# Kernel tuning notes

Hardware: AMD Instinct MI355X
Metric: run time of the kernel (lower is better)

## Reference

```python
import jax, jax.numpy as jnp
import numpy as np

D_MODEL = 1024
NUM_HEAD = 16
BATCH = 2
SEQ = 2048
NEG_INF = -1e9  # matches masked_fill value in the original


def setup_inputs() -> dict:
    key = jax.random.key(0)
    k1, k2, k3, k4, k5 = jax.random.split(key, 5)
    scale = 1.0 / np.sqrt(D_MODEL)
    return {
        "x": jax.random.normal(k1, (BATCH, SEQ, D_MODEL), dtype=jnp.float32),
        "q_weight": jax.random.normal(k2, (D_MODEL, D_MODEL), dtype=jnp.float32) * scale,
        "k_weight": jax.random.normal(k3, (D_MODEL, D_MODEL), dtype=jnp.float32) * scale,
        "v_weight": jax.random.normal(k4, (D_MODEL, D_MODEL), dtype=jnp.float32) * scale,
        "o_weight": jax.random.normal(k5, (D_MODEL, D_MODEL), dtype=jnp.float32) * scale,
    }


def reference(x, q_weight, k_weight, v_weight, o_weight):
    b, s, d = x.shape
    h = NUM_HEAD
    dh = d // h
    # projections: weight layout is (d_out, d_in)
    q = jnp.einsum('bsd,ed->bse', x, q_weight).reshape(b, s, h, dh).transpose(0, 2, 1, 3)
    k = jnp.einsum('bsd,ed->bse', x, k_weight).reshape(b, s, h, dh).transpose(0, 2, 1, 3)
    v = jnp.einsum('bsd,ed->bse', x, v_weight).reshape(b, s, h, dh).transpose(0, 2, 1, 3)
    scores = jnp.einsum('bhqd,bhkd->bhqk', q, k) / jnp.sqrt(jnp.asarray(dh, x.dtype))
    causal = jnp.triu(jnp.ones((s, s), dtype=bool), k=1)  # True above diagonal -> masked
    scores = jnp.where(causal, jnp.asarray(NEG_INF, x.dtype), scores)
    attn = jax.nn.softmax(scores, axis=-1)
    out = jnp.einsum('bhqk,bhkd->bhqd', attn, v)          # [b,h,s,dh]
    out = out.transpose(0, 2, 1, 3).reshape(b, s, d)       # merge heads
    return jnp.einsum('bse,de->bsd', out, o_weight)
```

## Files before the change

kernel.cpp:

```cpp
#include <hip/hip_runtime.h>

typedef short bhalf8 __attribute__((ext_vector_type(8)));
typedef float floatx4 __attribute__((ext_vector_type(4)));

#define D_MODEL 1024
#define SEQ     2048
#define BATCH   2
#define NHEAD   16
#define DH      64

#define GLDS(g, l) __builtin_amdgcn_global_load_lds( \
    (const __attribute__((address_space(1))) void*)(g), \
    (__attribute__((address_space(3))) void*)(l), 16, 0, 0)

static __device__ __forceinline__ short f2bf(float f) {
    unsigned u = __builtin_bit_cast(unsigned, f);
    u = (u + 0x7fffu + ((u >> 16) & 1u)) >> 16;
    return (short)u;
}
static __device__ __forceinline__ unsigned pack2(float a, float b) {
    return (unsigned)(unsigned short)f2bf(a) | ((unsigned)(unsigned short)f2bf(b) << 16);
}

__global__ __launch_bounds__(256) void cast_x(const float* __restrict__ s,
                                              short* __restrict__ d) {
    int i = (blockIdx.x * 256 + threadIdx.x) * 8;
    float4 a = *(const float4*)(s + i);
    float4 b = *(const float4*)(s + i + 4);
    uint4 u = {pack2(a.x, a.y), pack2(a.z, a.w), pack2(b.x, b.y), pack2(b.z, b.w)};
    *(uint4*)(d + i) = u;
}

__global__ __launch_bounds__(256) void cast_w(const float* __restrict__ wq,
                                              const float* __restrict__ wk,
                                              const float* __restrict__ wv,
                                              const float* __restrict__ wo,
                                              short* __restrict__ dst) {
    const float* s = (blockIdx.y == 0) ? wq : (blockIdx.y == 1) ? wk
                   : (blockIdx.y == 2) ? wv : wo;
    size_t off = (size_t)blockIdx.y * (D_MODEL * D_MODEL);
    int i = (blockIdx.x * 256 + threadIdx.x) * 8;
    float4 a = *(const float4*)(s + i);
    float4 b = *(const float4*)(s + i + 4);
    uint4 u = {pack2(a.x, a.y), pack2(a.z, a.w), pack2(b.x, b.y), pack2(b.z, b.w)};
    *(uint4*)(dst + off + i) = u;
}

__global__ __launch_bounds__(256) void gemm_qkv(const short* __restrict__ A,
                                                const short* __restrict__ W,
                                                short* __restrict__ Qo,
                                                short* __restrict__ Ko,
                                                short* __restrict__ Vt) {
    __shared__ __align__(16) char pool[34816];
    short (*As)[64] = (short(*)[64])pool;
    short (*Bs)[64] = (short(*)[64])(pool + 16384);
    const int t    = threadIdx.x;
    const int wave = t >> 6, lane = t & 63, quad = lane >> 4, l16 = lane & 15;
    const int bm = blockIdx.x * 128, by = blockIdx.y, bn = by * 128;
    const int qm = (wave >> 1) * 64, qn = (wave & 1) * 64;

    const int lrow = lane >> 3, lcol = (lane & 7) * 8;
    const short* Ag = A + (size_t)(bm + wave * 32 + lrow) * 1024 + lcol;
    const short* Wg = W + (size_t)(bn + wave * 32 + lrow) * 1024 + lcol;
    short* Al = &As[wave * 32][0];
    short* Bl = &Bs[wave * 32][0];

    floatx4 acc[4][4];
#pragma unroll
    for (int i = 0; i < 4; ++i)
#pragma unroll
        for (int j = 0; j < 4; ++j) {
            floatx4 z = {0.f, 0.f, 0.f, 0.f};
            acc[i][j] = z;
        }

    for (int k0 = 0; k0 < 1024; k0 += 64) {
        __syncthreads();
#pragma unroll
        for (int j = 0; j < 4; ++j) {
            GLDS(Ag + k0 + (size_t)j * 8 * 1024, Al + j * 8 * 64);
            GLDS(Wg + k0 + (size_t)j * 8 * 1024, Bl + j * 8 * 64);
        }
        __syncthreads();
#pragma unroll
        for (int kk = 0; kk < 64; kk += 32) {
            bhalf8 af[4], bfr[4];
#pragma unroll
            for (int im = 0; im < 4; ++im)
                af[im] = *(const bhalf8*)&As[qm + im * 16 + l16][kk + quad * 8];
#pragma unroll
            for (int jn = 0; jn < 4; ++jn)
                bfr[jn] = *(const bhalf8*)&Bs[qn + jn * 16 + l16][kk + quad * 8];
#pragma unroll
            for (int im = 0; im < 4; ++im)
#pragma unroll
                for (int jn = 0; jn < 4; ++jn)
                    acc[im][jn] = __builtin_amdgcn_mfma_f32_16x16x32_bf16(
                        af[im], bfr[jn], acc[im][jn], 0, 0, 0);
        }
    }

    __syncthreads();
    short (*Ct)[136] = (short(*)[136])pool;
    const bool isV = (by >= 16);
#pragma unroll
    for (int im = 0; im < 4; ++im)
#pragma unroll
        for (int jn = 0; jn < 4; ++jn)
#pragma unroll
            for (int g = 0; g < 4; ++g) {
                const int ml = qm + im * 16 + quad * 4 + g;
                const int nl = qn + jn * 16 + l16;
                if (isV) Ct[nl][ml] = f2bf(acc[im][jn][g]);
                else     Ct[ml][nl] = f2bf(acc[im][jn][g]);
            }
    __syncthreads();

    short* outp;
    size_t rowbase, colbase, stride;
    if (by < 8)       { outp = Qo; rowbase = bm;                colbase = bn;        stride = 1024; }
    else if (by < 16) { outp = Ko; rowbase = bm;                colbase = bn - 1024; stride = 1024; }
    else              { outp = Vt; rowbase = (size_t)bn - 2048; colbase = bm;        stride = 4096; }
#pragma unroll
    for (int pass = 0; pass < 8; ++pass) {
        const int r = (t >> 4) + pass * 16;
        const int c = (t & 15) * 8;
        uint4 u = *(const uint4*)&Ct[r][c];
        *(uint4*)(outp + (rowbase + r) * stride + colbase + c) = u;
    }
}

__global__ __launch_bounds__(256) void gemm_o(const short* __restrict__ A,
                                              const short* __restrict__ W,
                                              float* __restrict__ C) {
    __shared__ __align__(16) char pool[34816];
    short (*As)[64] = (short(*)[64])pool;
    short (*Bs)[64] = (short(*)[64])(pool + 16384);
    const int t    = threadIdx.x;
    const int wave = t >> 6, lane = t & 63, quad = lane >> 4, l16 = lane & 15;
    const int bm = blockIdx.x * 128, bn = blockIdx.y * 64;
    const int qm = (wave >> 1) * 64, qn = (wave & 1) * 32;

    const int lrow = lane >> 3, lcol = (lane & 7) * 8;
    const short* Ag = A + (size_t)(bm + wave * 32 + lrow) * 1024 + lcol;
    const short* Wg = W + (size_t)(bn + wave * 16 + lrow) * 1024 + lcol;
    short* Al = &As[wave * 32][0];
    short* Bl = &Bs[wave * 16][0];

    floatx4 acc[4][2];
#pragma unroll
    for (int i = 0; i < 4; ++i)
#pragma unroll
        for (int j = 0; j < 2; ++j) {
            floatx4 z = {0.f, 0.f, 0.f, 0.f};
            acc[i][j] = z;
        }

    for (int k0 = 0; k0 < 1024; k0 += 64) {
        __syncthreads();
#pragma unroll
        for (int j = 0; j < 4; ++j)
            GLDS(Ag + k0 + (size_t)j * 8 * 1024, Al + j * 8 * 64);
#pragma unroll
        for (int j = 0; j < 2; ++j)
            GLDS(Wg + k0 + (size_t)j * 8 * 1024, Bl + j * 8 * 64);
        __syncthreads();
#pragma unroll
        for (int kk = 0; kk < 64; kk += 32) {
            bhalf8 af[4], bfr[2];
#pragma unroll
            for (int im = 0; im < 4; ++im)
                af[im] = *(const bhalf8*)&As[qm + im * 16 + l16][kk + quad * 8];
#pragma unroll
            for (int jn = 0; jn < 2; ++jn)
                bfr[jn] = *(const bhalf8*)&Bs[qn + jn * 16 + l16][kk + quad * 8];
#pragma unroll
            for (int im = 0; im < 4; ++im)
#pragma unroll
                for (int jn = 0; jn < 2; ++jn)
                    acc[im][jn] = __builtin_amdgcn_mfma_f32_16x16x32_bf16(
                        af[im], bfr[jn], acc[im][jn], 0, 0, 0);
        }
    }

    __syncthreads();
    float (*Ctf)[68] = (float(*)[68])pool;
#pragma unroll
    for (int im = 0; im < 4; ++im)
#pragma unroll
        for (int jn = 0; jn < 2; ++jn)
#pragma unroll
            for (int g = 0; g < 4; ++g)
                Ctf[qm + im * 16 + quad * 4 + g][qn + jn * 16 + l16] = acc[im][jn][g];
    __syncthreads();
#pragma unroll
    for (int pass = 0; pass < 8; ++pass) {
        const int r = (t >> 4) + pass * 16;
        const int c = (t & 15) * 4;
        float4 u = *(const float4*)&Ctf[r][c];
        *(float4*)(C + (size_t)(bm + r) * 1024 + bn + c) = u;
    }
}

__global__ __launch_bounds__(512) void attn_v7(const short* __restrict__ Qo,
                                               const short* __restrict__ Ko,
                                               const short* __restrict__ Vt,
                                               short* __restrict__ Y) {
    __shared__ __align__(16) short Ps[8][32][72];
    const int t    = threadIdx.x;
    const int wave = t >> 6, lane = t & 63, quad = lane >> 4, l16 = lane & 15;
    const int bh = blockIdx.x, b = bh >> 4, h = bh & 15;
    const int qtile = (wave < 4) ? (15 - (int)blockIdx.y) : (int)blockIdx.y;
    const int qw = qtile * 128 + (wave & 3) * 32;

    const short* Qbase = Qo + (size_t)b * SEQ * 1024 + h * 64;
    const short* Kbase = Ko + (size_t)b * SEQ * 1024 + h * 64;
    const short* Vbase = Vt + (size_t)h * 64 * 4096 + (size_t)b * SEQ;

    bhalf8 qf[2][2];
#pragma unroll
    for (int im = 0; im < 2; ++im) {
        const short* qr = Qbase + (size_t)(qw + im * 16 + l16) * 1024;
        qf[im][0] = *(const bhalf8*)(qr + quad * 8);
        qf[im][1] = *(const bhalf8*)(qr + 32 + quad * 8);
    }

    float lsum[2][4];
    floatx4 o[2][4];
#pragma unroll
    for (int im = 0; im < 2; ++im)
#pragma unroll
        for (int g = 0; g < 4; ++g) lsum[im][g] = 0.f;
#pragma unroll
    for (int im = 0; im < 2; ++im)
#pragma unroll
        for (int nd = 0; nd < 4; ++nd) {
            floatx4 z = {0.f, 0.f, 0.f, 0.f};
            o[im][nd] = z;
        }

    const float KS = 0.125f * 1.44269504f;
    const float CB = 12.0f * 1.44269504f;

    for (int k0 = 0; k0 < qw + 32; k0 += 64) {
        bhalf8 kf[4][2];
#pragma unroll
        for (int jn = 0; jn < 4; ++jn) {
            const short* kr = Kbase + (size_t)(k0 + jn * 16 + l16) * 1024 + quad * 8;
            kf[jn][0] = *(const bhalf8*)(kr);
            kf[jn][1] = *(const bhalf8*)(kr + 32);
        }
        bhalf8 vt[4][2];
#pragma unroll
        for (int nd = 0; nd < 4; ++nd) {
            const short* vr = Vbase + (size_t)(nd * 16 + l16) * 4096 + k0 + quad * 8;
            vt[nd][0] = *(const bhalf8*)(vr);
            vt[nd][1] = *(const bhalf8*)(vr + 32);
        }

        floatx4 s[2][4];
#pragma unroll
        for (int im = 0; im < 2; ++im)
#pragma unroll
            for (int jn = 0; jn < 4; ++jn) {
                floatx4 z = {0.f, 0.f, 0.f, 0.f};
                z = __builtin_amdgcn_mfma_f32_16x16x32_bf16(qf[im][0], kf[jn][0], z, 0, 0, 0);
                z = __builtin_amdgcn_mfma_f32_16x16x32_bf16(qf[im][1], kf[jn][1], z, 0, 0, 0);
                s[im][jn] = z;
            }

        const bool partial = (k0 + 64 > qw);
#pragma unroll
        for (int im = 0; im < 2; ++im)
#pragma unroll
            for (int g = 0; g < 4; ++g) {
                const int rr = im * 16 + quad * 4 + g;
                const int qrow = qw + rr;
                float e0 = exp2f(s[im][0][g] * KS - CB);
                float e1 = exp2f(s[im][1][g] * KS - CB);
                float e2 = exp2f(s[im][2][g] * KS - CB);
                float e3 = exp2f(s[im][3][g] * KS - CB);
                if (partial) {
                    if (k0 + l16 > qrow)      e0 = 0.f;
                    if (k0 + 16 + l16 > qrow) e1 = 0.f;
                    if (k0 + 32 + l16 > qrow) e2 = 0.f;
                    if (k0 + 48 + l16 > qrow) e3 = 0.f;
                }
                lsum[im][g] += (e0 + e1) + (e2 + e3);
                Ps[wave][rr][l16]      = f2bf(e0);
                Ps[wave][rr][16 + l16] = f2bf(e1);
                Ps[wave][rr][32 + l16] = f2bf(e2);
                Ps[wave][rr][48 + l16] = f2bf(e3);
            }

#pragma unroll
        for (int im = 0; im < 2; ++im) {
            bhalf8 ap0 = *(const bhalf8*)&Ps[wave][im * 16 + l16][quad * 8];
            bhalf8 ap1 = *(const bhalf8*)&Ps[wave][im * 16 + l16][32 + quad * 8];
#pragma unroll
            for (int nd = 0; nd < 4; ++nd) {
                o[im][nd] = __builtin_amdgcn_mfma_f32_16x16x32_bf16(ap0, vt[nd][0], o[im][nd], 0, 0, 0);
                o[im][nd] = __builtin_amdgcn_mfma_f32_16x16x32_bf16(ap1, vt[nd][1], o[im][nd], 0, 0, 0);
            }
        }
    }

    float inv[2][4];
#pragma unroll
    for (int im = 0; im < 2; ++im)
#pragma unroll
        for (int g = 0; g < 4; ++g) {
            float r = lsum[im][g];
            r += __shfl_xor(r, 1, 64);
            r += __shfl_xor(r, 2, 64);
            r += __shfl_xor(r, 4, 64);
            r += __shfl_xor(r, 8, 64);
            inv[im][g] = 1.0f / r;
        }
#pragma unroll
    for (int im = 0; im < 2; ++im)
#pragma unroll
        for (int nd = 0; nd < 4; ++nd)
#pragma unroll
            for (int g = 0; g < 4; ++g) {
                const int qrow = qw + im * 16 + quad * 4 + g;
                Y[(size_t)(b * SEQ + qrow) * 1024 + h * 64 + nd * 16 + l16] =
                    f2bf(o[im][nd][g] * inv[im][g]);
            }
}

extern "C" void kernel_launch(void* const* d_in, const int* in_sizes, int n_in,
                              void* d_out, int out_size, void* d_ws, size_t ws_size,
                              hipStream_t stream) {
    const float* x  = (const float*)d_in[0];
    const float* wq = (const float*)d_in[1];
    const float* wk = (const float*)d_in[2];
    const float* wv = (const float*)d_in[3];
    const float* wo = (const float*)d_in[4];

    short* xb   = (short*)d_ws;
    short* Qo   = xb + (size_t)4096 * 1024;
    short* Ko   = Qo + (size_t)4096 * 1024;
    short* Vt   = Ko + (size_t)4096 * 1024;
    short* wall = Vt + (size_t)1024 * 4096;
    short* wob  = wall + (size_t)3 * 1024 * 1024;

    cast_x<<<dim3(2048), 256, 0, stream>>>(x, xb);
    cast_w<<<dim3(512, 4), 256, 0, stream>>>(wq, wk, wv, wo, wall);
    gemm_qkv<<<dim3(32, 24), 256, 0, stream>>>(xb, wall, Qo, Ko, Vt);
    attn_v7<<<dim3(BATCH * NHEAD, 8), 512, 0, stream>>>(Qo, Ko, Vt, xb);
    gemm_o<<<dim3(32, 16), 256, 0, stream>>>(xb, wob, (float*)d_out);
}
```

Measured before the change: 220.8 us.

## Rebalance causal attention work across waves with split-K merge and prefetching

Each wave pair now handles a high and a low 32-row query strip. Waves A process the first 17 key chunks of the high strip. Waves B process the low strip plus the remaining chunks of the high strip, and partial outputs and sums are merged through shared memory. This evens out per-wave causal work, which was skewed before. K/V fragments are also prefetched one chunk ahead, and bf16 packing uses the hardware cvt_pk instruction. The costs are extra register pressure, a block-wide sync with an LDS combine, and more complex indexing.

Measured after the change: 221.9 us. Within noise of the previous version (+0.5%).

```diff
diff --git a/kernel.cpp b/kernel.cpp
--- a/kernel.cpp
+++ b/kernel.cpp
@@ -20,6 +20,11 @@
 }
 static __device__ __forceinline__ unsigned pack2(float a, float b) {
     return (unsigned)(unsigned short)f2bf(a) | ((unsigned)(unsigned short)f2bf(b) << 16);
+}
+static __device__ __forceinline__ unsigned cvt_pk_bf16(float lo, float hi) {
+    unsigned r;
+    asm("v_cvt_pk_bf16_f32 %0, %1, %2" : "=v"(r) : "v"(lo), "v"(hi));
+    return r;
 }
 
 __global__ __launch_bounds__(256) void cast_x(const float* __restrict__ s,
@@ -202,131 +207,215 @@
     }
 }
 
-__global__ __launch_bounds__(512) void attn_v7(const short* __restrict__ Qo,
+#define LOADQ(qf, qwv) do {                                                   \
+    _Pragma("unroll")                                                         \
+    for (int im_ = 0; im_ < 2; ++im_) {                                       \
+        const short* qr_ = Qbase + (size_t)((qwv) + im_ * 16 + l16) * 1024;   \
+        qf[im_][0] = *(const bhalf8*)(qr_ + quad * 8);                        \
+        qf[im_][1] = *(const bhalf8*)(qr_ + 32 + quad * 8);                   \
+    } } while (0)
+
+#define LOADK(dst, kk) do {                                                   \
+    _Pragma("unroll")                                                         \
+    for (int jn_ = 0; jn_ < 4; ++jn_) {                                       \
+        const short* kr_ = Kbase + (size_t)((kk) + jn_ * 16 + l16) * 1024 + quad * 8; \
+        dst[jn_][0] = *(const bhalf8*)(kr_);                                  \
+        dst[jn_][1] = *(const bhalf8*)(kr_ + 32);                             \
+    } } while (0)
+
+#define LOADV(dst, kk) do {                                                   \
+    _Pragma("unroll")                                                         \
+    for (int nd_ = 0; nd_ < 4; ++nd_) {                                       \
+        const short* vr_ = Vbase + (size_t)(nd_ * 16 + l16) * 4096 + (kk) + quad * 8; \
+        dst[nd_][0] = *(const bhalf8*)(vr_);                                  \
+        dst[nd_][1] = *(const bhalf8*)(vr_ + 32);                             \
+    } } while (0)
+
+#define ZERO_ACC() do {                                                       \
+    _Pragma("unroll")                                                         \
+    for (int im_ = 0; im_ < 2; ++im_) {                                       \
+        _Pragma("unroll")                                                     \
+        for (int g_ = 0; g_ < 4; ++g_) lsum[im_][g_] = 0.f;                   \
+        _Pragma("unroll")                                                     \
+        for (int nd_ = 0; nd_ < 4; ++nd_) {                                   \
+            floatx4 z_ = {0.f, 0.f, 0.f, 0.f};                                \
+            o[im_][nd_] = z_;                                                 \
+        }                                                                     \
+    } } while (0)
+
+#define CHUNK(k0v, knv, qf, qwv) do {                                         \
+    floatx4 s_[2][4];                                                         \
+    _Pragma("unroll")                                                         \
+    for (int im_ = 0; im_ < 2; ++im_)                                         \
+        _Pragma("unroll")                                                     \
+        for (int jn_ = 0; jn_ < 4; ++jn_) {                                   \
+            floatx4 z_ = {0.f, 0.f, 0.f, 0.f};                                \
+            z_ = __builtin_amdgcn_mfma_f32_16x16x32_bf16(qf[im_][0], kf[jn_][0], z_, 0, 0, 0); \
+            z_ = __builtin_amdgcn_mfma_f32_16x16x32_bf16(qf[im_][1], kf[jn_][1], z_, 0, 0, 0); \
+            s_[im_][jn_] = z_;                                                \
+        }                                                                     \
+    LOADK(kf, knv);                                \
+    const bool partial_ = ((k0v) + 64 > (qwv));                               \
+    _Pragma("unroll")                                                         \
+    for (int im_ = 0; im_ < 2; ++im_)                                         \
+        _Pragma("unroll")                                                     \
+        for (int g_ = 0; g_ < 4; ++g_) {                                      \
+            const int rr_ = im_ * 16 + quad * 4 + g_;                         \
+            const int qrow_ = (qwv) + rr_;                                    \
+            float e0_ = exp2f(s_[im_][0][g_] * KS - CB);                      \
+            float e1_ = exp2f(s_[im_][1][g_] * KS - CB);                      \
+            float e2_ = exp2f(s_[im_][2][g_] * KS - CB);                      \
+            float e3_ = exp2f(s_[im_][3][g_] * KS - CB);                      \
+            if (partial_) {                                                   \
+                if ((k0v) + l16 > qrow_)      e0_ = 0.f;                      \
+                if ((k0v) + 16 + l16 > qrow_) e1_ = 0.f;                      \
+                if ((k0v) + 32 + l16 > qrow_) e2_ = 0.f;                      \
+                if ((k0v) + 48 + l16 > qrow_) e3_ = 0.f;                      \
+            }                                                                 \
+            lsum[im_][g_] += (e0_ + e1_) + (e2_ + e3_);                       \
+            unsigned r01_ = cvt_pk_bf16(e0_, e1_);                            \
+            unsigned r23_ = cvt_pk_bf16(e2_, e3_);                            \
+            Ps[wave][rr_][l16]      = (short)r01_;                            \
+            Ps[wave][rr_][16 + l16] = (short)(r01_ >> 16);                    \
+            Ps[wave][rr_][32 + l16] = (short)r23_;                            \
+            Ps[wave][rr_][48 + l16] = (short)(r23_ >> 16);                    \
+        }                                                                     \
+    _Pragma("unroll")                                                         \
+    for (int im_ = 0; im_ < 2; ++im_) {                                       \
+        bhalf8 ap0_ = *(const bhalf8*)&Ps[wave][im_ * 16 + l16][quad * 8];    \
+        bhalf8 ap1_ = *(const bhalf8*)&Ps[wave][im_ * 16 + l16][32 + quad * 8]; \
+        _Pragma("unroll")                                                     \
+        for (int nd_ = 0; nd_ < 4; ++nd_) {                                   \
+            o[im_][nd_] = __builtin_amdgcn_mfma_f32_16x16x32_bf16(ap0_, vt[nd_][0], o[im_][nd_], 0, 0, 0); \
+            o[im_][nd_] = __builtin_amdgcn_mfma_f32_16x16x32_bf16(ap1_, vt[nd_][1], o[im_][nd_], 0, 0, 0); \
+        }                                                                     \
+    }                                                                         \
+    LOADV(vt, knv);                                     \
+} while (0)
+
+#define RUN_SEG(nseg, kbase, qf, qwv) do {                                    \
+    const int n_ = (nseg);                                                    \
+    const int base_ = (kbase);                                                \
+    if (n_ > 0) {                                                             \
+        LOADK(kf, base_);                                                     \
+        LOADV(vt, base_);                                                     \
+        _Pragma("unroll 1")                                                   \
+        for (int i_ = 0; i_ < n_; ++i_) {                                     \
+            const int k0_ = base_ + i_ * 64;                                  \
+            const int kn_ = (i_ + 1 < n_) ? (k0_ + 64) : base_;               \
+            CHUNK(k0_, kn_, qf, qwv);                                         \
+        }                                                                     \
+    } } while (0)
+
+#define REDUCE_LSUM() do {                                                    \
+    _Pragma("unroll")                                                         \
+    for (int im_ = 0; im_ < 2; ++im_)                                         \
+        _Pragma("unroll")                                                     \
+        for (int g_ = 0; g_ < 4; ++g_) {                                      \
+            float r_ = lsum[im_][g_];                                         \
+            r_ += __shfl_xor(r_, 1, 64);                                      \
+            r_ += __shfl_xor(r_, 2, 64);                                      \
+            r_ += __shfl_xor(r_, 4, 64);                                      \
+            r_ += __shfl_xor(r_, 8, 64);                                      \
+            lsum[im_][g_] = r_;                                               \
+        } } while (0)
+
+#define STORE_OUT(qwv) do {                                                   \
+    _Pragma("unroll")                                                         \
+    for (int im_ = 0; im_ < 2; ++im_)                                         \
+        _Pragma("unroll")                                                     \
+        for (int g_ = 0; g_ < 4; ++g_) {                                      \
+            const float iv_ = 1.0f / lsum[im_][g_];                           \
+            const int qrow_ = (qwv) + im_ * 16 + quad * 4 + g_;               \
+            _Pragma("unroll")                                                 \
+            for (int nd_ = 0; nd_ < 4; ++nd_)                                 \
+                Y[(size_t)(b * SEQ + qrow_) * 1024 + h * 64 + nd_ * 16 + l16] = \
+                    f2bf(o[im_][nd_][g_] * iv_);                              \
+        } } while (0)
+
+__global__ __launch_bounds__(512) void attn_v8(const short* __restrict__ Qo,
                                                const short* __restrict__ Ko,
                                                const short* __restrict__ Vt,
                                                short* __restrict__ Y) {
-    __shared__ __align__(16) short Ps[8][32][72];
+    __shared__ __align__(16) char pool[45056];
+    short (*Ps)[32][72] = (short(*)[32][72])pool;
+    float (*Cmb)[44]    = (float(*)[44])pool;
+
     const int t    = threadIdx.x;
     const int wave = t >> 6, lane = t & 63, quad = lane >> 4, l16 = lane & 15;
     const int bh = blockIdx.x, b = bh >> 4, h = bh & 15;
-    const int qtile = (wave < 4) ? (15 - (int)blockIdx.y) : (int)blockIdx.y;
-    const int qw = qtile * 128 + (wave & 3) * 32;
+    const bool isA = (wave < 4);
+    const int j   = (int)blockIdx.y * 4 + (wave & 3);
+    const int sH  = 63 - j;
+    const int qwH = sH * 32, qwL = j * 32;
+    const int ncH = (65 - j) >> 1;
+    const int ncL = (j + 2) >> 1;
 
     const short* Qbase = Qo + (size_t)b * SEQ * 1024 + h * 64;
     const short* Kbase = Ko + (size_t)b * SEQ * 1024 + h * 64;
     const short* Vbase = Vt + (size_t)h * 64 * 4096 + (size_t)b * SEQ;
 
-    bhalf8 qf[2][2];
-#pragma unroll
-    for (int im = 0; im < 2; ++im) {
-        const short* qr = Qbase + (size_t)(qw + im * 16 + l16) * 1024;
-        qf[im][0] = *(const bhalf8*)(qr + quad * 8);
-        qf[im][1] = *(const bhalf8*)(qr + 32 + quad * 8);
-    }
-
+    const float KS = 0.125f * 1.44269504f;
+    const float CB = 12.0f * 1.44269504f;
+
+    bhalf8 kf[4][2], vt[4][2];
     float lsum[2][4];
     floatx4 o[2][4];
-#pragma unroll
-    for (int im = 0; im < 2; ++im)
-#pragma unroll
-        for (int g = 0; g < 4; ++g) lsum[im][g] = 0.f;
-#pragma unroll
-    for (int im = 0; im < 2; ++im)
-#pragma unroll
-        for (int nd = 0; nd < 4; ++nd) {
-            floatx4 z = {0.f, 0.f, 0.f, 0.f};
-            o[im][nd] = z;
-        }
-
-    const float KS = 0.125f * 1.44269504f;
-    const float CB = 12.0f * 1.44269504f;
-
-    for (int k0 = 0; k0 < qw + 32; k0 += 64) {
-        bhalf8 kf[4][2];
-#pragma unroll
-        for (int jn = 0; jn < 4; ++jn) {
-            const short* kr = Kbase + (size_t)(k0 + jn * 16 + l16) * 1024 + quad * 8;
-            kf[jn][0] = *(const bhalf8*)(kr);
-            kf[jn][1] = *(const bhalf8*)(kr + 32);
-        }
-        bhalf8 vt[4][2];
-#pragma unroll
-        for (int nd = 0; nd < 4; ++nd) {
-            const short* vr = Vbase + (size_t)(nd * 16 + l16) * 4096 + k0 + quad * 8;
-            vt[nd][0] = *(const bhalf8*)(vr);
-            vt[nd][1] = *(const bhalf8*)(vr + 32);
-        }
-
-        floatx4 s[2][4];
+    ZERO_ACC();
+
+    if (isA) {
+        bhalf8 qfH[2][2];
+        LOADQ(qfH, qwH);
+        RUN_SEG(17, 0, qfH, qwH);
+        REDUCE_LSUM();
+    } else {
+        {
+            bhalf8 qfL[2][2];
+            LOADQ(qfL, qwL);
+            RUN_SEG(ncL, 0, qfL, qwL);
+            REDUCE_LSUM();
+            STORE_OUT(qwL);
+        }
+        ZERO_ACC();
+        {
+            bhalf8 qfH[2][2];
+            LOADQ(qfH, qwH);
+            RUN_SEG(ncH - 17, 1088, qfH, qwH);
+            REDUCE_LSUM();
+        }
+    }
+
+    __syncthreads();
+    if (!isA) {
+        float* cp = &Cmb[(wave - 4) * 64 + lane][0];
 #pragma unroll
         for (int im = 0; im < 2; ++im)
 #pragma unroll
-            for (int jn = 0; jn < 4; ++jn) {
-                floatx4 z = {0.f, 0.f, 0.f, 0.f};
-                z = __builtin_amdgcn_mfma_f32_16x16x32_bf16(qf[im][0], kf[jn][0], z, 0, 0, 0);
-                z = __builtin_amdgcn_mfma_f32_16x16x32_bf16(qf[im][1], kf[jn][1], z, 0, 0, 0);
-                s[im][jn] = z;
+            for (int nd = 0; nd < 4; ++nd)
+                *(floatx4*)(cp + (im * 4 + nd) * 4) = o[im][nd];
+#pragma unroll
+        for (int im = 0; im < 2; ++im)
+#pragma unroll
+            for (int g = 0; g < 4; ++g)
+                cp[32 + im * 4 + g] = lsum[im][g];
+    }
+    __syncthreads();
+    if (isA) {
+        const float* cp = &Cmb[wave * 64 + lane][0];
+#pragma unroll
+        for (int im = 0; im < 2; ++im)
+#pragma unroll
+            for (int nd = 0; nd < 4; ++nd) {
+                floatx4 add = *(const floatx4*)(cp + (im * 4 + nd) * 4);
+                o[im][nd] += add;
             }
-
-        const bool partial = (k0 + 64 > qw);
 #pragma unroll
         for (int im = 0; im < 2; ++im)
 #pragma unroll
-            for (int g = 0; g < 4; ++g) {
-                const int rr = im * 16 + quad * 4 + g;
-                const int qrow = qw + rr;
-                float e0 = exp2f(s[im][0][g] * KS - CB);
-                float e1 = exp2f(s[im][1][g] * KS - CB);
-                float e2 = exp2f(s[im][2][g] * KS - CB);
-                float e3 = exp2f(s[im][3][g] * KS - CB);
-                if (partial) {
-                    if (k0 + l16 > qrow)      e0 = 0.f;
-                    if (k0 + 16 + l16 > qrow) e1 = 0.f;
-                    if (k0 + 32 + l16 > qrow) e2 = 0.f;
-                    if (k0 + 48 + l16 > qrow) e3 = 0.f;
-                }
-                lsum[im][g] += (e0 + e1) + (e2 + e3);
-                Ps[wave][rr][l16]      = f2bf(e0);
-                Ps[wave][rr][16 + l16] = f2bf(e1);
-                Ps[wave][rr][32 + l16] = f2bf(e2);
-                Ps[wave][rr][48 + l16] = f2bf(e3);
-            }
-
-#pragma unroll
-        for (int im = 0; im < 2; ++im) {
-            bhalf8 ap0 = *(const bhalf8*)&Ps[wave][im * 16 + l16][quad * 8];
-            bhalf8 ap1 = *(const bhalf8*)&Ps[wave][im * 16 + l16][32 + quad * 8];
-#pragma unroll
-            for (int nd = 0; nd < 4; ++nd) {
-                o[im][nd] = __builtin_amdgcn_mfma_f32_16x16x32_bf16(ap0, vt[nd][0], o[im][nd], 0, 0, 0);
-                o[im][nd] = __builtin_amdgcn_mfma_f32_16x16x32_bf16(ap1, vt[nd][1], o[im][nd], 0, 0, 0);
-            }
-        }
-    }
-
-    float inv[2][4];
-#pragma unroll
-    for (int im = 0; im < 2; ++im)
-#pragma unroll
-        for (int g = 0; g < 4; ++g) {
-            float r = lsum[im][g];
-            r += __shfl_xor(r, 1, 64);
-            r += __shfl_xor(r, 2, 64);
-            r += __shfl_xor(r, 4, 64);
-            r += __shfl_xor(r, 8, 64);
-            inv[im][g] = 1.0f / r;
-        }
-#pragma unroll
-    for (int im = 0; im < 2; ++im)
-#pragma unroll
-        for (int nd = 0; nd < 4; ++nd)
-#pragma unroll
-            for (int g = 0; g < 4; ++g) {
-                const int qrow = qw + im * 16 + quad * 4 + g;
-                Y[(size_t)(b * SEQ + qrow) * 1024 + h * 64 + nd * 16 + l16] =
-                    f2bf(o[im][nd][g] * inv[im][g]);
-            }
+            for (int g = 0; g < 4; ++g)
+                lsum[im][g] += cp[32 + im * 4 + g];
+        STORE_OUT(qwH);
+    }
 }
 
 extern "C" void kernel_launch(void* const* d_in, const int* in_sizes, int n_in,
@@ -348,6 +437,6 @@
     cast_x<<<dim3(2048), 256, 0, stream>>>(x, xb);
     cast_w<<<dim3(512, 4), 256, 0, stream>>>(wq, wk, wv, wo, wall);
     gemm_qkv<<<dim3(32, 24), 256, 0, stream>>>(xb, wall, Qo, Ko, Vt);
-    attn_v7<<<dim3(BATCH * NHEAD, 8), 512, 0, stream>>>(Qo, Ko, Vt, xb);
+    attn_v8<<<dim3(BATCH * NHEAD, 8), 512, 0, stream>>>(Qo, Ko, Vt, xb);
     gemm_o<<<dim3(32, 16), 256, 0, stream>>>(xb, wob, (float*)d_out);
 }
```

## Stage K/V tiles in double-buffered LDS shared by all waves in attention

Applied to the files above, without the earlier changes.

The attention kernel is restructured so that each block's 8 waves cooperatively load each 64-key K and V chunk into double-buffered shared memory, with register prefetch two chunks ahead. Before, every wave read K and V directly from global memory. Each wave now handles 16 query rows instead of 32, and the block processes two query tiles one after the other (a long one and a short one) to balance causal work. The probability packing uses the hardware v_cvt_pk_bf16_f32 instruction. In exchange, the kernel adds a barrier per chunk and lowers per-wave MFMA reuse of K and V fragments.

New measurement: 204.2 us. -7.5%, faster.

```diff
diff --git a/kernel.cpp b/kernel.cpp
--- a/kernel.cpp
+++ b/kernel.cpp
@@ -20,6 +20,11 @@
 }
 static __device__ __forceinline__ unsigned pack2(float a, float b) {
     return (unsigned)(unsigned short)f2bf(a) | ((unsigned)(unsigned short)f2bf(b) << 16);
+}
+static __device__ __forceinline__ unsigned cvt_pk_bf16(float lo, float hi) {
+    unsigned r;
+    asm("v_cvt_pk_bf16_f32 %0, %1, %2" : "=v"(r) : "v"(lo), "v"(hi));
+    return r;
 }
 
 __global__ __launch_bounds__(256) void cast_x(const float* __restrict__ s,
@@ -202,131 +207,143 @@
     }
 }
 
-__global__ __launch_bounds__(512) void attn_v7(const short* __restrict__ Qo,
-                                               const short* __restrict__ Ko,
-                                               const short* __restrict__ Vt,
-                                               short* __restrict__ Y) {
-    __shared__ __align__(16) short Ps[8][32][72];
+#define MFMA_BF16 __builtin_amdgcn_mfma_f32_16x16x32_bf16
+
+#define STAGE_LOAD(kregv, vregv, kk) do {                                     \
+    kregv = *(const uint4*)(Kbase + (size_t)((kk) + sr) * 1024 + sc);         \
+    vregv = *(const uint4*)(Vbase + (size_t)sr * 4096 + (kk) + sc);           \
+    } while (0)
+
+#define STAGE_WRITE(bufv, kregv, vregv) do {                                  \
+    *(uint4*)&Ks[bufv][sr][sc] = kregv;                                       \
+    *(uint4*)&Vs[bufv][sr][sc] = vregv;                                       \
+    } while (0)
+
+#define CHUNK13(bufv, k0v, qwv) do {                                          \
+    bhalf8 kf_[4][2];                                                         \
+    _Pragma("unroll")                                                         \
+    for (int jn_ = 0; jn_ < 4; ++jn_) {                                       \
+        kf_[jn_][0] = *(const bhalf8*)&Ks[bufv][jn_ * 16 + l16][quad * 8];    \
+        kf_[jn_][1] = *(const bhalf8*)&Ks[bufv][jn_ * 16 + l16][32 + quad * 8]; \
+    }                                                                         \
+    floatx4 s_[4];                                                            \
+    _Pragma("unroll")                                                         \
+    for (int jn_ = 0; jn_ < 4; ++jn_) {                                       \
+        floatx4 z_ = {0.f, 0.f, 0.f, 0.f};                                    \
+        z_ = MFMA_BF16(qf0, kf_[jn_][0], z_, 0, 0, 0);                        \
+        z_ = MFMA_BF16(qf1, kf_[jn_][1], z_, 0, 0, 0);                        \
+        s_[jn_] = z_;                                                         \
+    }                                                                         \
+    bhalf8 vf_[4][2];              \
+    _Pragma("unroll")                                                         \
+    for (int nd_ = 0; nd_ < 4; ++nd_) {                                       \
+        vf_[nd_][0] = *(const bhalf8*)&Vs[bufv][nd_ * 16 + l16][quad * 8];    \
+        vf_[nd_][1] = *(const bhalf8*)&Vs[bufv][nd_ * 16 + l16][32 + quad * 8]; \
+    }                                                                         \
+    const bool partial_ = ((k0v) + 64 > (qwv));                               \
+    _Pragma("unroll")                                                         \
+    for (int g_ = 0; g_ < 4; ++g_) {                                          \
+        const int rr_ = quad * 4 + g_;                                        \
+        const int qrow_ = (qwv) + rr_;                                        \
+        float e0_ = exp2f(s_[0][g_] * KS - CB);                               \
+        float e1_ = exp2f(s_[1][g_] * KS - CB);                               \
+        float e2_ = exp2f(s_[2][g_] * KS - CB);                               \
+        float e3_ = exp2f(s_[3][g_] * KS - CB);                               \
+        if (partial_) {                                                       \
+            if ((k0v) + l16 > qrow_)      e0_ = 0.f;                          \
+            if ((k0v) + 16 + l16 > qrow_) e1_ = 0.f;                          \
+            if ((k0v) + 32 + l16 > qrow_) e2_ = 0.f;                          \
+            if ((k0v) + 48 + l16 > qrow_) e3_ = 0.f;                          \
+        }                                                                     \
+        lsum[g_] += (e0_ + e1_) + (e2_ + e3_);                                \
+        unsigned r01_ = cvt_pk_bf16(e0_, e1_);                                \
+        unsigned r23_ = cvt_pk_bf16(e2_, e3_);                                \
+        Ps[wave][rr_][l16]      = (short)r01_;                                \
+        Ps[wave][rr_][16 + l16] = (short)(r01_ >> 16);                        \
+        Ps[wave][rr_][32 + l16] = (short)r23_;                                \
+        Ps[wave][rr_][48 + l16] = (short)(r23_ >> 16);                        \
+    }                                                                         \
+          \
+    bhalf8 ap0_ = *(const bhalf8*)&Ps[wave][l16][quad * 8];                   \
+    bhalf8 ap1_ = *(const bhalf8*)&Ps[wave][l16][32 + quad * 8];              \
+    _Pragma("unroll")                                                         \
+    for (int nd_ = 0; nd_ < 4; ++nd_) {                                       \
+        o[nd_] = MFMA_BF16(ap0_, vf_[nd_][0], o[nd_], 0, 0, 0);               \
+        o[nd_] = MFMA_BF16(ap1_, vf_[nd_][1], o[nd_], 0, 0, 0);               \
+    }                                                                         \
+} while (0)
+
+#define SWEEP(qtv, ncv) do {                                                  \
+    const int qw_ = (qtv) * 128 + wave * 16;                                  \
+    const short* qr_ = Qbase + (size_t)(qw_ + l16) * 1024;                    \
+    bhalf8 qf0 = *(const bhalf8*)(qr_ + quad * 8);                            \
+    bhalf8 qf1 = *(const bhalf8*)(qr_ + 32 + quad * 8);                       \
+    _Pragma("unroll")                                                         \
+    for (int g_ = 0; g_ < 4; ++g_) lsum[g_] = 0.f;                            \
+    _Pragma("unroll")                                                         \
+    for (int nd_ = 0; nd_ < 4; ++nd_) {                                       \
+        floatx4 z_ = {0.f, 0.f, 0.f, 0.f};                                    \
+        o[nd_] = z_;                                                          \
+    }                                                                         \
+    uint4 kreg_, vreg_;                                                       \
+    STAGE_LOAD(kreg_, vreg_, 0);                                              \
+    STAGE_WRITE(0, kreg_, vreg_);                                             \
+    if ((ncv) > 1) STAGE_LOAD(kreg_, vreg_, 64);                              \
+    __syncthreads();                                                          \
+    _Pragma("unroll 1")                                                       \
+    for (int i_ = 0; i_ < (ncv); ++i_) {                                      \
+        const int buf_ = i_ & 1;                                              \
+        if (i_ + 1 < (ncv)) STAGE_WRITE(buf_ ^ 1, kreg_, vreg_);              \
+        if (i_ + 2 < (ncv)) STAGE_LOAD(kreg_, vreg_, (i_ + 2) * 64);          \
+        CHUNK13(buf_, i_ * 64, qw_);                                          \
+        __syncthreads();                                                      \
+    }                                                                         \
+    _Pragma("unroll")                                                         \
+    for (int g_ = 0; g_ < 4; ++g_) {                                          \
+        float r_ = lsum[g_];                                                  \
+        r_ += __shfl_xor(r_, 1, 64);                                          \
+        r_ += __shfl_xor(r_, 2, 64);                                          \
+        r_ += __shfl_xor(r_, 4, 64);                                          \
+        r_ += __shfl_xor(r_, 8, 64);                                          \
+        const float iv_ = 1.0f / r_;                                          \
+        const int qrow_ = qw_ + quad * 4 + g_;                                \
+        _Pragma("unroll")                                                     \
+        for (int nd_ = 0; nd_ < 4; ++nd_)                                     \
+            Y[(size_t)(b * SEQ + qrow_) * 1024 + h * 64 + nd_ * 16 + l16] =   \
+                f2bf(o[nd_][g_] * iv_);                                       \
+    }                                                                         \
+} while (0)
+
+__global__ __launch_bounds__(512) void attn_v13(const short* __restrict__ Qo,
+                                                const short* __restrict__ Ko,
+                                                const short* __restrict__ Vt,
+                                                short* __restrict__ Y) {
+    __shared__ __align__(16) short Ks[2][64][72];
+    __shared__ __align__(16) short Vs[2][64][72];
+    __shared__ __align__(16) short Ps[8][16][72];
+
     const int t    = threadIdx.x;
     const int wave = t >> 6, lane = t & 63, quad = lane >> 4, l16 = lane & 15;
-    const int bh = blockIdx.x, b = bh >> 4, h = bh & 15;
-    const int qtile = (wave < 4) ? (15 - (int)blockIdx.y) : (int)blockIdx.y;
-    const int qw = qtile * 128 + (wave & 3) * 32;
+    const int bid  = (int)blockIdx.x;
+    const int bh   = bid & 31, pair = bid >> 5;
+    const int b = bh >> 4, h = bh & 15;
+    const int qtA = 15 - pair, qtB = pair;
 
     const short* Qbase = Qo + (size_t)b * SEQ * 1024 + h * 64;
     const short* Kbase = Ko + (size_t)b * SEQ * 1024 + h * 64;
     const short* Vbase = Vt + (size_t)h * 64 * 4096 + (size_t)b * SEQ;
 
-    bhalf8 qf[2][2];
-#pragma unroll
-    for (int im = 0; im < 2; ++im) {
-        const short* qr = Qbase + (size_t)(qw + im * 16 + l16) * 1024;
-        qf[im][0] = *(const bhalf8*)(qr + quad * 8);
-        qf[im][1] = *(const bhalf8*)(qr + 32 + quad * 8);
-    }
-
-    float lsum[2][4];
-    floatx4 o[2][4];
-#pragma unroll
-    for (int im = 0; im < 2; ++im)
-#pragma unroll
-        for (int g = 0; g < 4; ++g) lsum[im][g] = 0.f;
-#pragma unroll
-    for (int im = 0; im < 2; ++im)
-#pragma unroll
-        for (int nd = 0; nd < 4; ++nd) {
-            floatx4 z = {0.f, 0.f, 0.f, 0.f};
-            o[im][nd] = z;
-        }
+    const int sr = t >> 3;
+    const int sc = (t & 7) * 8;
 
     const float KS = 0.125f * 1.44269504f;
     const float CB = 12.0f * 1.44269504f;
 
-    for (int k0 = 0; k0 < qw + 32; k0 += 64) {
-        bhalf8 kf[4][2];
-#pragma unroll
-        for (int jn = 0; jn < 4; ++jn) {
-            const short* kr = Kbase + (size_t)(k0 + jn * 16 + l16) * 1024 + quad * 8;
-            kf[jn][0] = *(const bhalf8*)(kr);
-            kf[jn][1] = *(const bhalf8*)(kr + 32);
-        }
-        bhalf8 vt[4][2];
-#pragma unroll
-        for (int nd = 0; nd < 4; ++nd) {
-            const short* vr = Vbase + (size_t)(nd * 16 + l16) * 4096 + k0 + quad * 8;
-            vt[nd][0] = *(const bhalf8*)(vr);
-            vt[nd][1] = *(const bhalf8*)(vr + 32);
-        }
-
-        floatx4 s[2][4];
-#pragma unroll
-        for (int im = 0; im < 2; ++im)
-#pragma unroll
-            for (int jn = 0; jn < 4; ++jn) {
-                floatx4 z = {0.f, 0.f, 0.f, 0.f};
-                z = __builtin_amdgcn_mfma_f32_16x16x32_bf16(qf[im][0], kf[jn][0], z, 0, 0, 0);
-                z = __builtin_amdgcn_mfma_f32_16x16x32_bf16(qf[im][1], kf[jn][1], z, 0, 0, 0);
-                s[im][jn] = z;
-            }
-
-        const bool partial = (k0 + 64 > qw);
-#pragma unroll
-        for (int im = 0; im < 2; ++im)
-#pragma unroll
-            for (int g = 0; g < 4; ++g) {
-                const int rr = im * 16 + quad * 4 + g;
-                const int qrow = qw + rr;
-                float e0 = exp2f(s[im][0][g] * KS - CB);
-                float e1 = exp2f(s[im][1][g] * KS - CB);
-                float e2 = exp2f(s[im][2][g] * KS - CB);
-                float e3 = exp2f(s[im][3][g] * KS - CB);
-                if (partial) {
-                    if (k0 + l16 > qrow)      e0 = 0.f;
-                    if (k0 + 16 + l16 > qrow) e1 = 0.f;
-                    if (k0 + 32 + l16 > qrow) e2 = 0.f;
-                    if (k0 + 48 + l16 > qrow) e3 = 0.f;
-                }
-                lsum[im][g] += (e0 + e1) + (e2 + e3);
-                Ps[wave][rr][l16]      = f2bf(e0);
-                Ps[wave][rr][16 + l16] = f2bf(e1);
-                Ps[wave][rr][32 + l16] = f2bf(e2);
-                Ps[wave][rr][48 + l16] = f2bf(e3);
-            }
-
-#pragma unroll
-        for (int im = 0; im < 2; ++im) {
-            bhalf8 ap0 = *(const bhalf8*)&Ps[wave][im * 16 + l16][quad * 8];
-            bhalf8 ap1 = *(const bhalf8*)&Ps[wave][im * 16 + l16][32 + quad * 8];
-#pragma unroll
-            for (int nd = 0; nd < 4; ++nd) {
-                o[im][nd] = __builtin_amdgcn_mfma_f32_16x16x32_bf16(ap0, vt[nd][0], o[im][nd], 0, 0, 0);
-                o[im][nd] = __builtin_amdgcn_mfma_f32_16x16x32_bf16(ap1, vt[nd][1], o[im][nd], 0, 0, 0);
-            }
-        }
-    }
-
-    float inv[2][4];
-#pragma unroll
-    for (int im = 0; im < 2; ++im)
-#pragma unroll
-        for (int g = 0; g < 4; ++g) {
-            float r = lsum[im][g];
-            r += __shfl_xor(r, 1, 64);
-            r += __shfl_xor(r, 2, 64);
-            r += __shfl_xor(r, 4, 64);
-            r += __shfl_xor(r, 8, 64);
-            inv[im][g] = 1.0f / r;
-        }
-#pragma unroll
-    for (int im = 0; im < 2; ++im)
-#pragma unroll
-        for (int nd = 0; nd < 4; ++nd)
-#pragma unroll
-            for (int g = 0; g < 4; ++g) {
-                const int qrow = qw + im * 16 + quad * 4 + g;
-                Y[(size_t)(b * SEQ + qrow) * 1024 + h * 64 + nd * 16 + l16] =
-                    f2bf(o[im][nd][g] * inv[im][g]);
-            }
+    float lsum[4];
+    floatx4 o[4];
+
+    SWEEP(qtA, (qtA + 1) * 2);
+    SWEEP(qtB, (qtB + 1) * 2);
 }
 
 extern "C" void kernel_launch(void* const* d_in, const int* in_sizes, int n_in,
@@ -348,6 +365,6 @@
     cast_x<<<dim3(2048), 256, 0, stream>>>(x, xb);
     cast_w<<<dim3(512, 4), 256, 0, stream>>>(wq, wk, wv, wo, wall);
     gemm_qkv<<<dim3(32, 24), 256, 0, stream>>>(xb, wall, Qo, Ko, Vt);
-    attn_v7<<<dim3(BATCH * NHEAD, 8), 512, 0, stream>>>(Qo, Ko, Vt, xb);
+    attn_v13<<<dim3(256), 512, 0, stream>>>(Qo, Ko, Vt, xb);
     gemm_o<<<dim3(32, 16), 256, 0, stream>>>(xb, wob, (float*)d_out);
 }
```
